# Optimization experiments

Measured on AMD Instinct MI355X. Metric: run time of the kernel, lower is better.

## Reference

```python
import jax, jax.numpy as jnp
import numpy as np

IMAGE_SIZE = 640
NUM_CLASSES = 80
MAX_BOXES = 100
SCORE_THR = 0.25
IOU_THR = 0.1
K_PRE = 256  # pre-NMS candidates per class (fixed-shape surrogate for tf.where filtering)
ANCHORS = np.array([[10,13],[16,30],[33,23],[30,61],[62,45],[59,119],
                    [116,90],[156,198],[373,326]], dtype=np.float32)


def setup_inputs() -> dict:
    key = jax.random.key(0)
    k5, k4, k3 = jax.random.split(key, 3)
    B = 16
    return {
        "p5": jax.random.normal(k5, (B, 20, 20, 255), dtype=jnp.float32),
        "p4": jax.random.normal(k4, (B, 40, 40, 255), dtype=jnp.float32),
        "p3": jax.random.normal(k3, (B, 80, 80, 255), dtype=jnp.float32),
    }


def _decode_layer(fm, anchors):
    # fm: [B, g, g, 3*(5+C)]; anchors: [3, 2] in input-image pixels
    B, g = fm.shape[0], fm.shape[1]
    ratio = IMAGE_SIZE / g
    fm = fm.reshape(B, g, g, 3, 5 + NUM_CLASSES)
    ctr = jax.nn.sigmoid(fm[..., :2])                      # [B,g,g,3,2]
    gx, gy = jnp.meshgrid(jnp.arange(g), jnp.arange(g))    # 'xy' indexing, same as tf
    offset = jnp.stack([gx, gy], axis=-1).astype(fm.dtype)[:, :, None, :]
    ctr = (ctr + offset) * ratio                           # pixel-space centers (x, y)
    # (anchor/ratio)*exp(t)*ratio == anchor*exp(t)
    sizes = jnp.exp(fm[..., 2:4]) * anchors                # pixel-space (w, h)
    conf = jax.nn.sigmoid(fm[..., 4:5])
    prob = jax.nn.sigmoid(fm[..., 5:])
    boxes = jnp.concatenate([ctr, sizes], axis=-1).reshape(B, -1, 4)
    scores = (conf * prob).reshape(B, -1, NUM_CLASSES)
    return boxes, scores


def _pairwise_iou(b):
    # b: [K, 4] in (x1, y1, x2, y2)
    x1, y1, x2, y2 = b[:, 0], b[:, 1], b[:, 2], b[:, 3]
    area = jnp.maximum(x2 - x1, 0.0) * jnp.maximum(y2 - y1, 0.0)
    iw = jnp.maximum(jnp.minimum(x2[:, None], x2[None, :]) - jnp.maximum(x1[:, None], x1[None, :]), 0.0)
    ih = jnp.maximum(jnp.minimum(y2[:, None], y2[None, :]) - jnp.maximum(y1[:, None], y1[None, :]), 0.0)
    inter = iw * ih
    union = area[:, None] + area[None, :] - inter
    return inter / jnp.maximum(union, 1e-9)


def _nms_class(boxes, scores):
    # boxes: [N,4], scores: [N] for one class of one image
    s = jnp.where(scores > SCORE_THR, scores, -1.0)
    top_s, top_i = jax.lax.top_k(s, K_PRE)        # score-sorted candidates
    cb = jnp.take(boxes, top_i, axis=0)           # [K_PRE, 4]
    iou = _pairwise_iou(cb)                       # [K_PRE, K_PRE]
    idx = jnp.arange(K_PRE)
    supp0 = top_s <= SCORE_THR                    # below-threshold slots start suppressed

    def body(i, supp):
        alive = ~supp[i]
        return supp | (alive & (iou[i] > IOU_THR) & (idx > i))

    supp = jax.lax.fori_loop(0, K_PRE, body, supp0)
    keep = ~supp
    # tf NMS caps output at MAX_BOXES per class (boxes are score-sorted)
    keep = keep & (jnp.cumsum(keep.astype(jnp.int32)) <= MAX_BOXES)
    kept_s = jnp.where(keep, top_s, -1.0)
    return kept_s, top_i


def _nms_image(boxes, scores):
    # boxes: [N,4], scores: [N,C]
    kept_s, top_i = jax.vmap(_nms_class, in_axes=(None, 1))(boxes, scores)  # [C,K],[C,K]
    flat_s = kept_s.reshape(-1)
    flat_i = top_i.reshape(-1)
    cls = jnp.repeat(jnp.arange(NUM_CLASSES), K_PRE)
    fs, fi = jax.lax.top_k(flat_s, MAX_BOXES)     # global top-k across all classes
    box_idx = flat_i[fi]
    valid = fs > 0.0                              # padded/suppressed slots carry -1
    out_boxes = jnp.where(valid[:, None], jnp.take(boxes, box_idx, axis=0), -1.0)
    out_scores = jnp.where(valid, fs, -1.0)
    out_labels = jnp.where(valid, cls[fi], -1).astype(jnp.int32)
    return out_boxes, out_scores, out_labels


def reference(p5, p4, p3):
    b5, s5 = _decode_layer(p5, ANCHORS[6:9])
    b4, s4 = _decode_layer(p4, ANCHORS[3:6])
    b3, s3 = _decode_layer(p3, ANCHORS[0:3])
    boxes = jnp.concatenate([b5, b4, b3], axis=1)   # [B, 25200, 4] (cx, cy, w, h)
    scores = jnp.concatenate([s5, s4, s3], axis=1)  # [B, 25200, 80]
    cx, cy, w, h = boxes[..., 0], boxes[..., 1], boxes[..., 2], boxes[..., 3]
    boxes = jnp.stack([cx - w / 2, cy - h / 2, cx + w / 2, cy + h / 2], axis=-1)
    return jax.vmap(_nms_image)(boxes, scores)      # ([B,100,4], [B,100], [B,100] int32)
```

## Files before the change

### kernel.cpp

```cpp
#include <hip/hip_runtime.h>
#include <cstdint>

#define NBOX 25200
#define NCLS 80
#define NIMG 16
#define KPRE 256
#define MAXB 100
#define SCORE_THR 0.25f
#define IOU_THR 0.1f
#define GCAP 512
#define GCAP_OLD 2048
#define NBINS_OLD 4096
#define FK 512
#define LCAP 3072
#define SCAP 24
#define CSTR 16
#define CUT 0.5f
#define BINW 0.001953125f
#define HS2 512.0f
#define RSC 262144.0f
#define BPI 394
#define FBBINS 2048

__constant__ float c_AW[9] = {10.f,16.f,33.f,30.f,62.f,59.f,116.f,156.f,373.f};
__constant__ float c_AH[9] = {13.f,30.f,23.f,61.f,45.f,119.f,90.f,198.f,326.f};

__device__ __forceinline__ float sigmoidf_(float x) { return 1.0f / (1.0f + expf(-x)); }

__device__ __forceinline__ void box_loc(int i, const float* p5, const float* p4, const float* p3,
                                        const float*& p, int& g, int& li, int& abase) {
  if (i < 1200)      { p = p5; g = 20; li = i;        abase = 6; }
  else if (i < 6000) { p = p4; g = 40; li = i - 1200; abase = 3; }
  else               { p = p3; g = 80; li = i - 6000; abase = 0; }
}

__device__ __forceinline__ float score_full(const float* p5, const float* p4, const float* p3,
                                            int b, int c, int i) {
  const float* p; int g, li, abase;
  box_loc(i, p5, p4, p3, p, g, li, abase);
  const float* f = p + (size_t)((size_t)b * g * g * 3 + li) * 85;
  return __fmul_rn(sigmoidf_(f[4]), sigmoidf_(f[5 + c]));
}

__global__ __launch_bounds__(512) void decode_push_kernel(
    const float* __restrict__ p5, const float* __restrict__ p4, const float* __restrict__ p3,
    float* __restrict__ boxes, unsigned long long* __restrict__ lists,
    uint32_t* __restrict__ cnts, uint32_t* __restrict__ ovfl)
{
  __shared__ float rec[64 * 85];
  __shared__ float conf_s[64];
  __shared__ unsigned long long slist[NCLS][SCAP];
  __shared__ uint32_t wcnt[NCLS];
  __shared__ uint32_t sbase[NCLS], sst[NCLS];
  __shared__ unsigned short pairbuf[8 * 64];

  const int bi = blockIdx.x;
  const int b = bi / BPI, r = bi - b * BPI;
  const float* p; int g, lb, s0, nb, abase;
  if (r < 19)      { p = p5; g = 20; lb = 0;    s0 = r * 64;        abase = 6; nb = 1200  - s0; }
  else if (r < 94) { p = p4; g = 40; lb = 1200; s0 = (r - 19) * 64; abase = 3; nb = 4800  - s0; }
  else             { p = p3; g = 80; lb = 6000; s0 = (r - 94) * 64; abase = 0; nb = 19200 - s0; }
  if (nb > 64) nb = 64;
  const int tid = threadIdx.x;

  if (tid < NCLS) wcnt[tid] = 0;
  {
    const float4* src4 = (const float4*)(p + ((size_t)b * g * g * 3 + s0) * 85);
    float4* rec4 = (float4*)rec;
    int n4 = nb * 85 / 4;
    int full = n4 >> 6;
    const int wave = tid >> 6, lane = tid & 63;
    for (int ch = wave; ch < full; ch += 8) {
      int base = ch << 6;
      __builtin_amdgcn_global_load_lds(
          (const __attribute__((address_space(1))) void*)(uintptr_t)(src4 + base + lane),
          (__attribute__((address_space(3))) void*)(uintptr_t)(rec4 + base + lane),
          16, 0, 0);
    }
    for (int k = (full << 6) + tid; k < n4; k += 512) rec4[k] = src4[k];
  }
  __syncthreads();

  if (tid < nb) {
    const float* f = rec + tid * 85;
    int li = s0 + tid;
    int cell = li / 3, a = li - cell * 3;
    float ratio = 640.0f / (float)g;
    float cx = (sigmoidf_(f[0]) + (float)(cell % g)) * ratio;
    float cy = (sigmoidf_(f[1]) + (float)(cell / g)) * ratio;
    float w = expf(f[2]) * c_AW[abase + a];
    float h = expf(f[3]) * c_AH[abase + a];
    float hw = 0.5f * w, hh = 0.5f * h;
    float4* ob = (float4*)(boxes + ((size_t)b * NBOX + lb + li) * 4);
    *ob = make_float4(cx - hw, cy - hh, cx + hw, cy + hh);
    conf_s[tid] = sigmoidf_(f[4]);
  }
  __syncthreads();

  {
    const int wave = tid >> 6, lane = tid & 63;
    const int c0 = wave * 10;
    const bool jok = lane < nb;
    float cl = jok ? rec[lane * 85 + 4] : -1.0f;
    float Lthr;
    if (!jok || cl <= 0.0f) {
      Lthr = 3.0e38f;
    } else {
      float conf = conf_s[lane];
      float u2 = CUT / conf;
      if (u2 > 0.999f) Lthr = -3.0e38f;
      else Lthr = logf(u2 / (1.0f - u2)) - 0.01f;
    }
    const float* fl = rec + lane * 85 + 5;
    const unsigned long long lt = (lane == 0) ? 0ull : (~0ull >> (64 - lane));
    unsigned short* pb = pairbuf + (wave << 6);

    auto flushFn = [&](int mm) {
      if (lane < mm) {
        int e = pb[lane];
        int l2 = e >> 4, cc2 = e & 15;
        int c2 = c0 + cc2;
        float s = __fmul_rn(conf_s[l2], sigmoidf_(rec[l2 * 85 + 5 + c2]));
        if (s > CUT) {
          uint32_t slot = atomicAdd(&wcnt[c2], 1u);
          if (slot < SCAP)
            slist[c2][slot] = ((unsigned long long)__float_as_uint(s) << 32)
                              | (0xFFFFFFFFu - (uint32_t)(lb + s0 + l2));
        }
      }
    };

    int m = 0;
    for (int cc = 0; cc < 10; ++cc) {
      float lg = jok ? fl[c0 + cc] : -3.0e38f;
      bool cand = lg > Lthr;
      unsigned long long mk = __ballot(cand);
      int pc = __popcll(mk);
      if (m + pc > 64) { flushFn(m); m = 0; }
      if (cand) {
        int rank = __popcll(mk & lt);
        pb[m + rank] = (unsigned short)((lane << 4) | cc);
      }
      m += pc;
    }
    flushFn(m);
  }
  __syncthreads();

  if (tid < NCLS) {
    uint32_t full = wcnt[tid];
    if (full > SCAP) ovfl[b * NCLS + tid] = 1u;
    uint32_t st = full < SCAP ? full : SCAP;
    sst[tid] = st;
    sbase[tid] = atomicAdd(&cnts[(size_t)(b * NCLS + tid) * CSTR], st);
  }
  __syncthreads();

  for (int t = tid; t < NCLS * SCAP; t += 512) {
    int c = t / SCAP, k = t - c * SCAP;
    if ((uint32_t)k < sst[c]) {
      uint32_t dst = sbase[c] + (uint32_t)k;
      if (dst < LCAP)
        lists[(size_t)(b * NCLS + c) * LCAP + dst] = slist[c][k];
    }
  }
}

union ShMix2 {
  uint32_t rhist[512];
  uint32_t fhist[FBBINS];
  unsigned long long rowm[KPRE][4];
};

__global__ __launch_bounds__(512) void select_nms_list_kernel(
    const unsigned long long* __restrict__ lists, const uint32_t* __restrict__ cnts,
    const uint32_t* __restrict__ ovfl, const float* __restrict__ boxes,
    const float* __restrict__ p5, const float* __restrict__ p4, const float* __restrict__ p3,
    float* __restrict__ kept_s, int* __restrict__ top_i)
{
  const int task = blockIdx.x;
  const int b = task / NCLS, c = task - b * NCLS;
  const int tid = threadIdx.x;

  __shared__ uint32_t S[256];
  __shared__ unsigned long long keys[GCAP];
  __shared__ ShMix2 u;
  __shared__ float4 bbx[KPRE];
  __shared__ float bar_[KPRE];
  __shared__ unsigned long long suppInit[4];
  __shared__ unsigned long long sh_t[4];
  __shared__ int s_B, s_cnt, s_state, sh_stop;
  __shared__ float s_gl, s_lo, s_hi;
  __shared__ uint32_t s_above, s_g2;

  const uint32_t cntraw = cnts[(size_t)task * CSTR];
  bool fb = (ovfl[task] != 0u) || !(cntraw >= (uint32_t)KPRE && cntraw <= (uint32_t)LCAP);
  float thr = CUT;
  int n_all = (int)(cntraw < (uint32_t)LCAP ? cntraw : (uint32_t)LCAP);
  const unsigned long long* gl = lists + (size_t)task * LCAP;

  if (!fb && n_all > 500) {
    if (tid < 256) S[tid] = 0;
    __syncthreads();
    for (int z = tid; z < n_all; z += 512) {
      float s = __uint_as_float((uint32_t)(gl[z] >> 32));
      int bin = (int)(__fmul_rn(__fsub_rn(s, CUT), HS2));
      bin = bin < 0 ? 0 : (bin > 255 ? 255 : bin);
      atomicAdd(&S[bin], 1u);
    }
    __syncthreads();
    for (int off = 1; off < 256; off <<= 1) {
      uint32_t add = 0;
      if (tid < 256 && tid + off < 256) add = S[tid + off];
      __syncthreads();
      if (tid < 256) S[tid] += add;
      __syncthreads();
    }
    if (tid == 0) s_B = 0;
    __syncthreads();
    if (tid < 256) {
      uint32_t Sz = S[tid];
      uint32_t Sz1 = (tid < 255) ? S[tid + 1] : 0u;
      if (Sz >= KPRE && (tid == 255 || Sz1 < KPRE)) s_B = tid;
    }
    __syncthreads();
    const int B = s_B;
    const uint32_t gcount = S[B];
    const uint32_t aboveB = (B < 255) ? S[B + 1] : 0u;
    thr = CUT + (float)B * BINW;
    if (gcount > 500u) {
      for (int z = tid; z < 512; z += 512) u.rhist[z] = 0u;
      __syncthreads();
      float rLo = thr;
      for (int z = tid; z < n_all; z += 512) {
        float s = __uint_as_float((uint32_t)(gl[z] >> 32));
        int bin = (int)(__fmul_rn(__fsub_rn(s, CUT), HS2));
        bin = bin < 0 ? 0 : (bin > 255 ? 255 : bin);
        if (bin == B) {
          int sub = (int)((s - rLo) * RSC);
          sub = sub < 0 ? 0 : (sub > 511 ? 511 : sub);
          atomicAdd(&u.rhist[sub], 1u);
        }
      }
      __syncthreads();
      if (tid == 0) {
        uint32_t acc = aboveB; int B2 = 0;
        for (int z = 511; z >= 0; --z) {
          acc += u.rhist[z];
          if (acc >= KPRE) { B2 = z; break; }
        }
        s_gl = rLo + (float)B2 * (BINW / 512.0f);
        s_g2 = acc;
      }
      __syncthreads();
      thr = s_gl;
      if (s_g2 > 500u) fb = true;
      __syncthreads();
    }
  }

  if (fb) {
    float lo = SCORE_THR, hi = 1.0f;
    uint32_t above = 0;
    float gl2 = SCORE_THR;
    bool done = false;
    for (int iter = 0; iter < 6 && !done; ++iter) {
      for (int z = tid; z < FBBINS; z += 512) u.fhist[z] = 0u;
      __syncthreads();
      float scale = (float)FBBINS / (hi - lo);
      for (int i = tid; i < NBOX; i += 512) {
        float s = score_full(p5, p4, p3, b, c, i);
        if (s > lo && s <= hi) {
          int bin = (int)((s - lo) * scale);
          bin = bin < 0 ? 0 : (bin > FBBINS - 1 ? FBBINS - 1 : bin);
          atomicAdd(&u.fhist[bin], 1u);
        }
      }
      __syncthreads();
      if (tid < 256) {
        uint32_t cs = 0; int base = tid * 8;
        #pragma unroll
        for (int z = 0; z < 8; ++z) cs += u.fhist[base + z];
        S[tid] = cs;
      }
      __syncthreads();
      if (tid == 0) {
        uint32_t acc = 0; int ch;
        for (ch = 255; ch >= 0; --ch) {
          if (above + acc + S[ch] >= KPRE) break;
          acc += S[ch];
        }
        if (ch < 0) { s_state = 1; s_gl = SCORE_THR; }
        else {
          int B = -1;
          for (int z = ch * 8 + 7; z >= ch * 8; --z) {
            acc += u.fhist[z];
            if (above + acc >= KPRE) { B = z; break; }
          }
          uint32_t popB = u.fhist[B];
          uint32_t aboveNew = above + acc - popB;
          float wdt = (hi - lo) / (float)FBBINS;
          float binLo = lo + (float)B * wdt;
          if (aboveNew + popB <= 496u || iter == 5) { s_state = 1; s_gl = binLo; }
          else { s_state = 0; s_lo = binLo; s_hi = binLo + wdt; s_above = aboveNew; }
        }
      }
      __syncthreads();
      if (s_state == 1) { gl2 = s_gl; done = true; }
      else { lo = s_lo; hi = s_hi; above = s_above; }
      __syncthreads();
    }
    thr = gl2;
  }

  float thr_n = __uint_as_float(__float_as_uint(thr) - 8u);

  if (tid == 0) s_cnt = 0;
  __syncthreads();
  if (!fb) {
    for (int z = tid; z < n_all; z += 512) {
      unsigned long long kk = gl[z];
      float s = __uint_as_float((uint32_t)(kk >> 32));
      if (s > thr_n) {
        int slot = atomicAdd(&s_cnt, 1);
        if (slot < GCAP) keys[slot] = kk;
      }
    }
  } else {
    for (int i = tid; i < NBOX; i += 512) {
      float s = score_full(p5, p4, p3, b, c, i);
      if (s > thr_n && s > SCORE_THR) {
        int slot = atomicAdd(&s_cnt, 1);
        if (slot < GCAP)
          keys[slot] = ((unsigned long long)__float_as_uint(s) << 32) | (0xFFFFFFFFu - (uint32_t)i);
      }
    }
  }
  __syncthreads();
  int n = s_cnt < GCAP ? s_cnt : GCAP;
  if (tid >= n) keys[tid] = 0ull;
  __syncthreads();
  {
    unsigned long long v = keys[tid];
    for (int k = 2; k <= GCAP; k <<= 1) {
      for (int j = k >> 1; j > 0; j >>= 1) {
        unsigned long long pv;
        if (j >= 64) {
          keys[tid] = v;
          __syncthreads();
          pv = keys[tid ^ j];
          __syncthreads();
        } else {
          pv = __shfl_xor(v, j, 64);
        }
        bool takeMax = (((tid & k) == 0) == ((tid & j) == 0));
        v = takeMax ? (v > pv ? v : pv) : (v < pv ? v : pv);
      }
    }
    keys[tid] = v;
  }
  __syncthreads();

  const int col = tid & 255;
  float sc; int idx;
  {
    unsigned long long kk = keys[col];
    if ((uint32_t)(kk >> 32) != 0u) { sc = __uint_as_float((uint32_t)(kk >> 32)); idx = (int)(0xFFFFFFFFu - (uint32_t)kk); }
    else { sc = -1.0f; idx = 0; }
  }
  if (tid < KPRE) {
    const float* bp = boxes + ((size_t)b * NBOX + idx) * 4;
    float bx1 = bp[0], by1 = bp[1], bx2 = bp[2], by2 = bp[3];
    bbx[tid] = make_float4(bx1, by1, bx2, by2);
    bar_[tid] = __fmul_rn(fmaxf(__fsub_rn(bx2, bx1), 0.0f), fmaxf(__fsub_rn(by2, by1), 0.0f));
  }
  {
    unsigned long long alive = __ballot(sc > SCORE_THR);
    if (tid < KPRE && (tid & 63) == 0) suppInit[tid >> 6] = ~alive;
  }
  if (tid == 0) sh_stop = 0;
  __syncthreads();
  float4 MB = bbx[col];
  float x1 = MB.x, y1 = MB.y, x2 = MB.z, y2 = MB.w;
  float area = bar_[col];
  if (tid < 4) sh_t[tid] = suppInit[tid];
  __syncthreads();

  int P = 4;
  const int rg = tid >> 8;
  #pragma unroll
  for (int q = 0; q < 4; ++q) {
    for (int ii = 0; ii < 64; ii += 2) {
      int i = q * 64 + ii + rg;
      if (!((sh_t[q] >> (ii + rg)) & 1ull)) {
        float4 B = bbx[i];
        float ar = bar_[i];
        float iw = fmaxf(__fsub_rn(fminf(x2, B.z), fmaxf(x1, B.x)), 0.0f);
        float ih = fmaxf(__fsub_rn(fminf(y2, B.w), fmaxf(y1, B.y)), 0.0f);
        float inter = __fmul_rn(iw, ih);
        float ab = __fadd_rn(ar, area);
        float diff = __fsub_rn(__fmul_rn(inter, 1.1f), __fmul_rn(0.1f, ab));
        bool sup;
        if (fabsf(diff) > 1e-5f * ab) {
          sup = diff > 0.0f;
        } else {
          float uni = __fsub_rn(ab, inter);
          sup = (inter / fmaxf(uni, 1e-9f)) > IOU_THR;
        }
        sup = sup && (col > i);
        unsigned long long m = __ballot(sup);
        if ((tid & 63) == 0) u.rowm[i][(tid >> 6) & 3] = m;
      }
    }
    __syncthreads();
    if (tid == 0) {
      unsigned long long t0 = sh_t[0], t1 = sh_t[1], t2 = sh_t[2], t3 = sh_t[3];
      for (int ii = 0; ii < 64; ++ii) {
        int i = q * 64 + ii;
        unsigned long long cur = (q == 0) ? t0 : (q == 1) ? t1 : (q == 2) ? t2 : t3;
        if (!((cur >> ii) & 1ull)) {
          if (q <= 0) t0 |= u.rowm[i][0];
          if (q <= 1) t1 |= u.rowm[i][1];
          if (q <= 2) t2 |= u.rowm[i][2];
          t3 |= u.rowm[i][3];
        }
      }
      sh_t[0] = t0; sh_t[1] = t1; sh_t[2] = t2; sh_t[3] = t3;
      int kept = __popcll(~t0);
      if (q >= 1) kept += __popcll(~t1);
      if (q >= 2) kept += __popcll(~t2);
      if (q >= 3) kept += __popcll(~t3);
      if (kept >= MAXB) sh_stop = 1;
    }
    __syncthreads();
    if (sh_stop) { P = q + 1; break; }
  }

  if (tid < KPRE) {
    unsigned long long tw = sh_t[tid >> 6];
    bool kept = (tid < 64 * P) && !((tw >> (tid & 63)) & 1ull);
    int rank = 0;
    #pragma unroll
    for (int w2 = 0; w2 < 4; ++w2)
      if (w2 < (tid >> 6)) rank += __popcll(~sh_t[w2]);
    int l = tid & 63;
    rank += (l == 0) ? 0 : __popcll(~tw & ((~0ull) >> (64 - l)));
    bool fin = kept && (rank < MAXB);
    kept_s[(size_t)task * KPRE + tid] = fin ? sc : -1.0f;
    top_i[(size_t)task * KPRE + tid] = idx;
  }
}

__global__ __launch_bounds__(256) void decode_kernel(
    const float* __restrict__ p5, const float* __restrict__ p4, const float* __restrict__ p3,
    float* __restrict__ boxes, float* __restrict__ conf)
{
  int t = blockIdx.x * 256 + threadIdx.x;
  if (t >= NIMG * NBOX) return;
  int b = t / NBOX, i = t - b * NBOX;
  const float* p; int g, li, abase;
  box_loc(i, p5, p4, p3, p, g, li, abase);
  int cell = li / 3, a = li - cell * 3;
  float ratio = 640.0f / (float)g;
  const float* f = p + ((size_t)((size_t)b * g * g + cell) * 255 + a * 85);
  float cx = (sigmoidf_(f[0]) + (float)(cell % g)) * ratio;
  float cy = (sigmoidf_(f[1]) + (float)(cell / g)) * ratio;
  float w = expf(f[2]) * c_AW[abase + a];
  float h = expf(f[3]) * c_AH[abase + a];
  float hw = 0.5f * w, hh = 0.5f * h;
  float* ob = boxes + (size_t)t * 4;
  ob[0] = cx - hw; ob[1] = cy - hh; ob[2] = cx + hw; ob[3] = cy + hh;
  conf[t] = sigmoidf_(f[4]);
}

__device__ __forceinline__ float score_at(
    const float* __restrict__ p5, const float* __restrict__ p4, const float* __restrict__ p3,
    const float* __restrict__ conf, int b, int c, int i)
{
  const float* p; int g, li, abase;
  box_loc(i, p5, p4, p3, p, g, li, abase);
  float logit = p[(size_t)((size_t)b * g * g * 3 + li) * 85 + 5 + c];
  return __fmul_rn(conf[b * NBOX + i], 1.0f / (1.0f + expf(-logit)));
}

__global__ __launch_bounds__(256) void select_nms_kernel(
    const float* __restrict__ p5, const float* __restrict__ p4, const float* __restrict__ p3,
    const float* __restrict__ conf, const float* __restrict__ boxes,
    float* __restrict__ kept_s, int* __restrict__ top_i)
{
  const int task = blockIdx.x;
  const int b = task / NCLS, c = task - b * NCLS;
  const int tid = threadIdx.x;
  __shared__ uint32_t hist[NBINS_OLD];
  __shared__ uint32_t chunkS[256];
  __shared__ unsigned long long keys[GCAP_OLD];
  __shared__ float s_lo, s_hi, s_glo;
  __shared__ uint32_t s_above;
  __shared__ int s_state, s_cnt;

  float lo = SCORE_THR, hi = 1.0f;
  uint32_t above = 0;
  float gatherLo = SCORE_THR;
  bool done = false;
  for (int iter = 0; iter < 6 && !done; ++iter) {
    for (int z = tid; z < NBINS_OLD; z += 256) hist[z] = 0;
    __syncthreads();
    float scale = (float)NBINS_OLD / (hi - lo);
    for (int i = tid; i < NBOX; i += 256) {
      float s = score_at(p5, p4, p3, conf, b, c, i);
      if (s > lo && s <= hi) {
        int bin = (int)((s - lo) * scale);
        bin = bin < 0 ? 0 : (bin > NBINS_OLD - 1 ? NBINS_OLD - 1 : bin);
        atomicAdd(&hist[bin], 1u);
      }
    }
    __syncthreads();
    { uint32_t cs = 0; int base = tid * 16;
      #pragma unroll
      for (int z = 0; z < 16; ++z) cs += hist[base + z];
      chunkS[tid] = cs; }
    __syncthreads();
    if (tid == 0) {
      uint32_t acc = 0; int ch;
      for (ch = 255; ch >= 0; --ch) {
        if (above + acc + chunkS[ch] >= KPRE) break;
        acc += chunkS[ch];
      }
      if (ch < 0) { s_state = 1; s_glo = SCORE_THR; }
      else {
        int B = -1;
        for (int z = ch * 16 + 15; z >= ch * 16; --z) {
          acc += hist[z];
          if (above + acc >= KPRE) { B = z; break; }
        }
        uint32_t popB = hist[B];
        uint32_t aboveNew = above + acc - popB;
        float wdt = (hi - lo) / (float)NBINS_OLD;
        float binLo = lo + (float)B * wdt;
        if (aboveNew + popB <= 1024u || iter == 5) { s_state = 1; s_glo = binLo; }
        else { s_state = 0; s_lo = binLo; s_hi = binLo + wdt; s_above = aboveNew; }
      }
    }
    __syncthreads();
    if (s_state == 1) { gatherLo = s_glo; done = true; }
    else { lo = s_lo; hi = s_hi; above = s_above; }
    __syncthreads();
  }
  gatherLo = __uint_as_float(__float_as_uint(gatherLo) - 8u);
  if (tid == 0) s_cnt = 0;
  __syncthreads();
  for (int i = tid; i < NBOX; i += 256) {
    float s = score_at(p5, p4, p3, conf, b, c, i);
    if (s > gatherLo && s > SCORE_THR) {
      int slot = atomicAdd(&s_cnt, 1);
      if (slot < GCAP_OLD)
        keys[slot] = ((unsigned long long)__float_as_uint(s) << 32) | (uint32_t)(0xFFFFFFFFu - (uint32_t)i);
    }
  }
  __syncthreads();
  int n = s_cnt < GCAP_OLD ? s_cnt : GCAP_OLD;
  for (int z = tid; z < GCAP_OLD; z += 256) if (z >= n) keys[z] = 0ull;
  __syncthreads();
  for (int k = 2; k <= GCAP_OLD; k <<= 1) {
    for (int j = k >> 1; j > 0; j >>= 1) {
      for (int i2 = tid; i2 < GCAP_OLD; i2 += 256) {
        int ixj = i2 ^ j;
        if (ixj > i2) {
          unsigned long long a0 = keys[i2], b0_ = keys[ixj];
          bool sw = ((i2 & k) == 0) ? (a0 < b0_) : (a0 > b0_);
          if (sw) { keys[i2] = b0_; keys[ixj] = a0; }
        }
      }
      __syncthreads();
    }
  }
  __shared__ float bx1[KPRE], by1[KPRE], bx2[KPRE], by2[KPRE], bar_[KPRE], tsc[KPRE];
  __shared__ int tix[KPRE];
  __shared__ unsigned char suppA[KPRE], keepA[KPRE];
  { int r = tid;
    unsigned long long kk = keys[r];
    float sc; int idx;
    if ((uint32_t)(kk >> 32) != 0u) { sc = __uint_as_float((uint32_t)(kk >> 32)); idx = (int)(0xFFFFFFFFu - (uint32_t)kk); }
    else { sc = -1.0f; idx = 0; }
    tsc[r] = sc; tix[r] = idx;
    const float* bp = boxes + ((size_t)b * NBOX + idx) * 4;
    float x1 = bp[0], y1 = bp[1], x2 = bp[2], y2 = bp[3];
    bx1[r] = x1; by1[r] = y1; bx2[r] = x2; by2[r] = y2;
    bar_[r] = __fmul_rn(fmaxf(__fsub_rn(x2, x1), 0.0f), fmaxf(__fsub_rn(y2, y1), 0.0f));
    suppA[r] = (sc <= SCORE_THR) ? 1 : 0; }
  __syncthreads();
  for (int i = 0; i < KPRE; ++i) {
    if (suppA[i] == 0) {
      int r = tid;
      if (r > i) {
        float iw = fmaxf(__fsub_rn(fminf(bx2[r], bx2[i]), fmaxf(bx1[r], bx1[i])), 0.0f);
        float ih = fmaxf(__fsub_rn(fminf(by2[r], by2[i]), fmaxf(by1[r], by1[i])), 0.0f);
        float inter = __fmul_rn(iw, ih);
        float uni = __fsub_rn(__fadd_rn(bar_[r], bar_[i]), inter);
        float iou = inter / fmaxf(uni, 1e-9f);
        if (iou > IOU_THR) suppA[r] = 1;
      }
    }
    __syncthreads();
  }
  if (tid == 0) {
    int cnt = 0;
    for (int r = 0; r < KPRE; ++r) {
      int kp = (suppA[r] == 0) ? 1 : 0;
      if (kp && cnt < MAXB) cnt++; else kp = 0;
      keepA[r] = (unsigned char)kp;
    }
  }
  __syncthreads();
  { int r = tid;
    kept_s[(size_t)task * KPRE + r] = keepA[r] ? tsc[r] : -1.0f;
    top_i[(size_t)task * KPRE + r] = tix[r]; }
}

__global__ __launch_bounds__(256) void final_topk_kernel(
    const float* __restrict__ kept_s, const int* __restrict__ top_i,
    const float* __restrict__ boxes, float* __restrict__ out)
{
  int b = blockIdx.x, tid = threadIdx.x;
  __shared__ uint32_t hist[NBINS_OLD];
  __shared__ uint32_t chunkS[256];
  __shared__ unsigned long long keys[FK];
  __shared__ float s_lo, s_hi, s_glo;
  __shared__ uint32_t s_above;
  __shared__ int s_state, s_cnt;
  const float* ks = kept_s + (size_t)b * NCLS * KPRE;
  const int NK = NCLS * KPRE;

  float lo = SCORE_THR, hi = 1.0f;
  uint32_t above = 0;
  float gatherLo = SCORE_THR;
  bool done = false;

  for (int iter = 0; iter < 4 && !done; ++iter) {
    for (int z = tid; z < NBINS_OLD; z += 256) hist[z] = 0;
    __syncthreads();
    float scale = (float)NBINS_OLD / (hi - lo);
    for (int z = tid; z < NK; z += 256) {
      float s = ks[z];
      if (s > lo && s <= hi) {
        int bin = (int)((s - lo) * scale);
        bin = bin < 0 ? 0 : (bin > NBINS_OLD - 1 ? NBINS_OLD - 1 : bin);
        atomicAdd(&hist[bin], 1u);
      }
    }
    __syncthreads();
    {
      uint32_t cs = 0; int base = tid * 16;
      #pragma unroll
      for (int z = 0; z < 16; ++z) cs += hist[base + z];
      chunkS[tid] = cs;
    }
    __syncthreads();
    if (tid == 0) {
      uint32_t acc = 0; int ch;
      for (ch = 255; ch >= 0; --ch) {
        if (above + acc + chunkS[ch] >= MAXB) break;
        acc += chunkS[ch];
      }
      if (ch < 0) { s_state = 1; s_glo = SCORE_THR; }
      else {
        int B = -1;
        for (int z = ch * 16 + 15; z >= ch * 16; --z) {
          acc += hist[z];
          if (above + acc >= MAXB) { B = z; break; }
        }
        uint32_t popB = hist[B];
        uint32_t aboveNew = above + acc - popB;
        float wdt = (hi - lo) / (float)NBINS_OLD;
        float binLo = lo + (float)B * wdt;
        if (aboveNew + popB <= (uint32_t)(FK - 64) || iter == 3) { s_state = 1; s_glo = binLo; }
        else { s_state = 0; s_lo = binLo; s_hi = binLo + wdt; s_above = aboveNew; }
      }
    }
    __syncthreads();
    if (s_state == 1) { gatherLo = s_glo; done = true; }
    else { lo = s_lo; hi = s_hi; above = s_above; }
    __syncthreads();
  }
  gatherLo = __uint_as_float(__float_as_uint(gatherLo) - 8u);

  if (tid == 0) s_cnt = 0;
  __syncthreads();
  for (int z = tid; z < NK; z += 256) {
    float s = ks[z];
    if (s > gatherLo && s > 0.0f) {
      int slot = atomicAdd(&s_cnt, 1);
      if (slot < FK)
        keys[slot] = ((unsigned long long)__float_as_uint(s) << 32) | (uint32_t)(0xFFFFFFFFu - (uint32_t)z);
    }
  }
  __syncthreads();
  int n = s_cnt < FK ? s_cnt : FK;
  for (int z = tid; z < FK; z += 256) if (z >= n) keys[z] = 0ull;
  __syncthreads();
  for (int k = 2; k <= FK; k <<= 1) {
    for (int j = k >> 1; j > 0; j >>= 1) {
      for (int i2 = tid; i2 < FK; i2 += 256) {
        int ixj = i2 ^ j;
        if (ixj > i2) {
          unsigned long long a0 = keys[i2], b0_ = keys[ixj];
          bool sw = ((i2 & k) == 0) ? (a0 < b0_) : (a0 > b0_);
          if (sw) { keys[i2] = b0_; keys[ixj] = a0; }
        }
      }
      __syncthreads();
    }
  }
  float* ob = out + (size_t)b * MAXB * 4;
  float* os = out + (size_t)NIMG * MAXB * 4 + (size_t)b * MAXB;
  float* ol = out + (size_t)NIMG * MAXB * 4 + (size_t)NIMG * MAXB + (size_t)b * MAXB;
  for (int t = tid; t < MAXB; t += 256) {
    unsigned long long kk = keys[t];
    if ((uint32_t)(kk >> 32) != 0u) {
      float s = __uint_as_float((uint32_t)(kk >> 32));
      int fr = (int)(0xFFFFFFFFu - (uint32_t)kk);
      int cc = fr >> 8, rr = fr & 255;
      int idx = top_i[((size_t)b * NCLS + cc) * KPRE + rr];
      const float* bp = boxes + ((size_t)b * NBOX + idx) * 4;
      ob[t * 4 + 0] = bp[0]; ob[t * 4 + 1] = bp[1]; ob[t * 4 + 2] = bp[2]; ob[t * 4 + 3] = bp[3];
      os[t] = s; ol[t] = (float)cc;
    } else {
      ob[t * 4 + 0] = -1.0f; ob[t * 4 + 1] = -1.0f; ob[t * 4 + 2] = -1.0f; ob[t * 4 + 3] = -1.0f;
      os[t] = -1.0f; ol[t] = -1.0f;
    }
  }
}

extern "C" void kernel_launch(void* const* d_in, const int* in_sizes, int n_in,
                              void* d_out, int out_size, void* d_ws, size_t ws_size,
                              hipStream_t stream)
{
  const float* p5 = (const float*)d_in[0];
  const float* p4 = (const float*)d_in[1];
  const float* p3 = (const float*)d_in[2];
  float* out = (float*)d_out;

  float*    boxes = (float*)d_ws;
  float*    kept  = boxes + (size_t)NIMG * NBOX * 4;
  int*      topi  = (int*)(kept + (size_t)NIMG * NCLS * KPRE);
  uint32_t* cnts  = (uint32_t*)(topi + (size_t)NIMG * NCLS * KPRE);
  uint32_t* ovfl  = cnts + (size_t)NIMG * NCLS * CSTR;
  unsigned long long* lists = (unsigned long long*)(ovfl + NIMG * NCLS);

  size_t need_main = ((size_t)NIMG * NBOX * 4 + (size_t)NIMG * NCLS * KPRE * 2
                      + (size_t)NIMG * NCLS * CSTR + (size_t)NIMG * NCLS) * 4
                     + (size_t)NIMG * NCLS * LCAP * 8;

  if (ws_size >= need_main) {
    hipMemsetAsync(cnts, 0, (size_t)NIMG * NCLS * (CSTR + 1) * sizeof(uint32_t), stream);
    decode_push_kernel<<<NIMG * BPI, 512, 0, stream>>>(p5, p4, p3, boxes, lists, cnts, ovfl);
    select_nms_list_kernel<<<NIMG * NCLS, 512, 0, stream>>>(lists, cnts, ovfl, boxes, p5, p4, p3, kept, topi);
  } else {
    float* conf = (float*)(cnts);
    decode_kernel<<<(NIMG * NBOX + 255) / 256, 256, 0, stream>>>(p5, p4, p3, boxes, conf);
    select_nms_kernel<<<NIMG * NCLS, 256, 0, stream>>>(p5, p4, p3, conf, boxes, kept, topi);
  }
  final_topk_kernel<<<NIMG, 256, 0, stream>>>(kept, topi, boxes, out);
}
```

Before: 207.1 us.

## Compact candidate boxes before class scan, use wave scans in NMS stages

In the decode kernel, boxes whose objectness logit is non-positive are dropped up front. The per-class scan then iterates only over (compacted box, class) pairs, so fewer iterations are spent on boxes that can never pass the cutoff. The 256-bin histogram prefix sum moves from a barrier-heavy block-wide loop to a single-wave shuffle scan. The serial single-thread NMS mask reduction becomes a one-wave loop that broadcasts row masks with shuffles instead of reading LDS, at the cost of extra index arithmetic and a divergence-dependent loop count.

Result: slower. 213.9 us (+3.3%).

```diff
diff --git a/kernel.cpp b/kernel.cpp
--- a/kernel.cpp
+++ b/kernel.cpp
@@ -49,13 +49,16 @@
 {
   __shared__ float rec[64 * 85];
   __shared__ float conf_s[64];
+  __shared__ float Lthr_s[64];
+  __shared__ unsigned char cbox[64];
+  __shared__ uint32_t mShared;
   __shared__ unsigned long long slist[NCLS][SCAP];
   __shared__ uint32_t wcnt[NCLS];
   __shared__ uint32_t sbase[NCLS], sst[NCLS];
   __shared__ unsigned short pairbuf[8 * 64];
 
-  const int bi = blockIdx.x;
-  const int b = bi / BPI, r = bi - b * BPI;
+  const int bi_ = blockIdx.x;
+  const int b = bi_ / BPI, r = bi_ - b * BPI;
   const float* p; int g, lb, s0, nb, abase;
   if (r < 19)      { p = p5; g = 20; lb = 0;    s0 = r * 64;        abase = 6; nb = 1200  - s0; }
   else if (r < 94) { p = p4; g = 40; lb = 1200; s0 = (r - 19) * 64; abase = 3; nb = 4800  - s0; }
@@ -81,69 +84,84 @@
   }
   __syncthreads();
 
-  if (tid < nb) {
-    const float* f = rec + tid * 85;
-    int li = s0 + tid;
-    int cell = li / 3, a = li - cell * 3;
-    float ratio = 640.0f / (float)g;
-    float cx = (sigmoidf_(f[0]) + (float)(cell % g)) * ratio;
-    float cy = (sigmoidf_(f[1]) + (float)(cell / g)) * ratio;
-    float w = expf(f[2]) * c_AW[abase + a];
-    float h = expf(f[3]) * c_AH[abase + a];
-    float hw = 0.5f * w, hh = 0.5f * h;
-    float4* ob = (float4*)(boxes + ((size_t)b * NBOX + lb + li) * 4);
-    *ob = make_float4(cx - hw, cy - hh, cx + hw, cy + hh);
-    conf_s[tid] = sigmoidf_(f[4]);
+  if (tid < 64) {
+    const bool in = tid < nb;
+    float cl = in ? rec[tid * 85 + 4] : -1.0f;
+    if (in) {
+      const float* f = rec + tid * 85;
+      int li = s0 + tid;
+      int cell = li / 3, a = li - cell * 3;
+      float ratio = 640.0f / (float)g;
+      float cx = (sigmoidf_(f[0]) + (float)(cell % g)) * ratio;
+      float cy = (sigmoidf_(f[1]) + (float)(cell / g)) * ratio;
+      float w = expf(f[2]) * c_AW[abase + a];
+      float h = expf(f[3]) * c_AH[abase + a];
+      float hw = 0.5f * w, hh = 0.5f * h;
+      float4* ob = (float4*)(boxes + ((size_t)b * NBOX + lb + li) * 4);
+      *ob = make_float4(cx - hw, cy - hh, cx + hw, cy + hh);
+      float conf = sigmoidf_(cl);
+      conf_s[tid] = conf;
+      float Lthr;
+      if (cl <= 0.0f) Lthr = 3.0e38f;
+      else {
+        float u2 = CUT / conf;
+        if (u2 > 0.999f) Lthr = -3.0e38f;
+        else Lthr = logf(u2 / (1.0f - u2)) - 0.01f;
+      }
+      Lthr_s[tid] = Lthr;
+    }
+    bool bok = in && cl > 0.0f;
+    unsigned long long mb = __ballot(bok);
+    if (bok) {
+      unsigned long long lt = (tid == 0) ? 0ull : (~0ull >> (64 - tid));
+      cbox[__popcll(mb & lt)] = (unsigned char)tid;
+    }
+    if (tid == 0) mShared = (uint32_t)__popcll(mb);
   }
   __syncthreads();
 
   {
     const int wave = tid >> 6, lane = tid & 63;
     const int c0 = wave * 10;
-    const bool jok = lane < nb;
-    float cl = jok ? rec[lane * 85 + 4] : -1.0f;
-    float Lthr;
-    if (!jok || cl <= 0.0f) {
-      Lthr = 3.0e38f;
-    } else {
-      float conf = conf_s[lane];
-      float u2 = CUT / conf;
-      if (u2 > 0.999f) Lthr = -3.0e38f;
-      else Lthr = logf(u2 / (1.0f - u2)) - 0.01f;
-    }
-    const float* fl = rec + lane * 85 + 5;
     const unsigned long long lt = (lane == 0) ? 0ull : (~0ull >> (64 - lane));
     unsigned short* pb = pairbuf + (wave << 6);
+    const int npairs = (int)mShared * 10;
 
     auto flushFn = [&](int mm) {
       if (lane < mm) {
         int e = pb[lane];
-        int l2 = e >> 4, cc2 = e & 15;
+        int b2 = e >> 4, cc2 = e & 15;
         int c2 = c0 + cc2;
-        float s = __fmul_rn(conf_s[l2], sigmoidf_(rec[l2 * 85 + 5 + c2]));
+        float s = __fmul_rn(conf_s[b2], sigmoidf_(rec[b2 * 85 + 5 + c2]));
         if (s > CUT) {
           uint32_t slot = atomicAdd(&wcnt[c2], 1u);
           if (slot < SCAP)
             slist[c2][slot] = ((unsigned long long)__float_as_uint(s) << 32)
-                              | (0xFFFFFFFFu - (uint32_t)(lb + s0 + l2));
+                              | (0xFFFFFFFFu - (uint32_t)(lb + s0 + b2));
         }
       }
     };
 
-    int m = 0;
-    for (int cc = 0; cc < 10; ++cc) {
-      float lg = jok ? fl[c0 + cc] : -3.0e38f;
-      bool cand = lg > Lthr;
+    int mp = 0;
+    for (int t = 0; t * 64 < npairs; ++t) {
+      int pr = t * 64 + lane;
+      bool valid = pr < npairs;
+      int q = (pr * 6554) >> 16;
+      int cc = pr - 10 * q;
+      int bx = valid ? (int)cbox[q] : 0;
+      float Lt = Lthr_s[bx];
+      float lg = valid ? rec[bx * 85 + 5 + c0 + cc] : -3.0e38f;
+      bool cand = valid && lg > Lt;
       unsigned long long mk = __ballot(cand);
       int pc = __popcll(mk);
-      if (m + pc > 64) { flushFn(m); m = 0; }
+      if (mp + pc > 64) { flushFn(mp); mp = 0; }
       if (cand) {
         int rank = __popcll(mk & lt);
-        pb[m + rank] = (unsigned short)((lane << 4) | cc);
-      }
-      m += pc;
-    }
-    flushFn(m);
+        pb[mp + rank] = (unsigned short)((bx << 4) | cc);
+      }
+      mp += pc;
+    }
+    flushFn(mp);
   }
   __syncthreads();
 
@@ -209,12 +227,20 @@
       atomicAdd(&S[bin], 1u);
     }
     __syncthreads();
-    for (int off = 1; off < 256; off <<= 1) {
-      uint32_t add = 0;
-      if (tid < 256 && tid + off < 256) add = S[tid + off];
-      __syncthreads();
-      if (tid < 256) S[tid] += add;
-      __syncthreads();
+    if (tid < 64) {
+      uint32_t v0 = S[tid * 4 + 0], v1 = S[tid * 4 + 1], v2 = S[tid * 4 + 2], v3 = S[tid * 4 + 3];
+      uint32_t s3 = v3, s2 = v2 + s3, s1 = v1 + s2, s0v = v0 + s1;
+      uint32_t acc = s0v;
+      #pragma unroll
+      for (int off = 1; off < 64; off <<= 1) {
+        int src = tid + off;
+        uint32_t o = __shfl(acc, src < 64 ? src : tid, 64);
+        if (src >= 64) o = 0u;
+        acc += o;
+      }
+      uint32_t hi2 = acc - s0v;
+      S[tid * 4 + 0] = s0v + hi2; S[tid * 4 + 1] = s1 + hi2;
+      S[tid * 4 + 2] = s2 + hi2;  S[tid * 4 + 3] = s3 + hi2;
     }
     if (tid == 0) s_B = 0;
     __syncthreads();
@@ -413,24 +439,28 @@
       }
     }
     __syncthreads();
-    if (tid == 0) {
+    if (tid < 64) {
+      unsigned long long r0 = u.rowm[q * 64 + tid][0];
+      unsigned long long r1 = u.rowm[q * 64 + tid][1];
+      unsigned long long r2 = u.rowm[q * 64 + tid][2];
+      unsigned long long r3 = u.rowm[q * 64 + tid][3];
       unsigned long long t0 = sh_t[0], t1 = sh_t[1], t2 = sh_t[2], t3 = sh_t[3];
+      unsigned long long tq = (q == 0) ? t0 : (q == 1) ? t1 : (q == 2) ? t2 : t3;
       for (int ii = 0; ii < 64; ++ii) {
-        int i = q * 64 + ii;
-        unsigned long long cur = (q == 0) ? t0 : (q == 1) ? t1 : (q == 2) ? t2 : t3;
-        if (!((cur >> ii) & 1ull)) {
-          if (q <= 0) t0 |= u.rowm[i][0];
-          if (q <= 1) t1 |= u.rowm[i][1];
-          if (q <= 2) t2 |= u.rowm[i][2];
-          t3 |= u.rowm[i][3];
-        }
-      }
-      sh_t[0] = t0; sh_t[1] = t1; sh_t[2] = t2; sh_t[3] = t3;
-      int kept = __popcll(~t0);
-      if (q >= 1) kept += __popcll(~t1);
-      if (q >= 2) kept += __popcll(~t2);
-      if (q >= 3) kept += __popcll(~t3);
-      if (kept >= MAXB) sh_stop = 1;
+        if (!((tq >> ii) & 1ull)) {
+          t0 |= __shfl(r0, ii, 64); t1 |= __shfl(r1, ii, 64);
+          t2 |= __shfl(r2, ii, 64); t3 |= __shfl(r3, ii, 64);
+          tq = (q == 0) ? t0 : (q == 1) ? t1 : (q == 2) ? t2 : t3;
+        }
+      }
+      if (tid == 0) {
+        sh_t[0] = t0; sh_t[1] = t1; sh_t[2] = t2; sh_t[3] = t3;
+        int kept = __popcll(~t0);
+        if (q >= 1) kept += __popcll(~t1);
+        if (q >= 2) kept += __popcll(~t2);
+        if (q >= 3) kept += __popcll(~t3);
+        if (kept >= MAXB) sh_stop = 1;
+      }
     }
     __syncthreads();
     if (sh_stop) { P = q + 1; break; }
```
